# Kernel tuning notes

Measured on AMD Instinct MI355X. Metric: run time of the kernel, lower is better.

## Reference

```python
import jax, jax.numpy as jnp
import numpy as np


def _inside_mask(points, boxes3d):
    # points: (B, N, 3); boxes3d: (B, M, 7) = (cx, cy, cz_bottom, dx, dy, dz, rz)
    cx, cy, cz, dx, dy, dz, rz = [boxes3d[..., i] for i in range(7)]
    cz = cz + dz * 0.5  # bottom-center -> geometric center (mmcv convention)
    # shift into box frame: (B, M, N)
    sx = points[:, None, :, 0] - cx[..., None]
    sy = points[:, None, :, 1] - cy[..., None]
    sz = points[:, None, :, 2] - cz[..., None]
    cosa = jnp.cos(-rz)[..., None]
    sina = jnp.sin(-rz)[..., None]
    lx = sx * cosa - sy * sina
    ly = sx * sina + sy * cosa
    return (
        (jnp.abs(lx) < dx[..., None] * 0.5)
        & (jnp.abs(ly) < dy[..., None] * 0.5)
        & (jnp.abs(sz) <= dz[..., None] * 0.5)
    )


def setup_inputs() -> dict:
    key = jax.random.key(0)
    k1, k2, k3 = jax.random.split(key, 3)
    B, N, M, C = 4, 16384, 128, 128
    points = jax.random.uniform(k1, (B, N, 3), dtype=jnp.float32)
    point_features = jax.random.normal(k2, (B, N, C), dtype=jnp.float32)
    boxes3d = jax.random.uniform(k3, (B, M, 7), dtype=jnp.float32)
    return {
        "points": points,
        "point_features": point_features,
        "boxes3d": boxes3d,
        "num_sampled_points": 512,
    }


def reference(points, point_features, boxes3d, num_sampled_points):
    S = num_sampled_points
    mask = _inside_mask(points, boxes3d)            # (B, M, N) bool
    cnt = mask.sum(axis=-1)                          # (B, M)
    # stable sort brings inside-point indices first, in original order
    order = jnp.argsort((~mask).astype(jnp.int32), axis=-1, stable=True)  # (B, M, N)
    cnt_safe = jnp.maximum(cnt, 1)
    # CUDA kernel: sample index k maps to k % cnt (== k when k < cnt)
    sample_pos = jnp.arange(S, dtype=cnt.dtype)[None, None, :] % cnt_safe[..., None]
    idx = jnp.take_along_axis(order, sample_pos, axis=-1)  # (B, M, S)
    gathered_pts = jnp.take_along_axis(points[:, None], idx[..., None], axis=2)          # (B, M, S, 3)
    gathered_feat = jnp.take_along_axis(point_features[:, None], idx[..., None], axis=2)  # (B, M, S, C)
    pooled = jnp.concatenate([gathered_pts, gathered_feat], axis=-1)  # (B, M, S, 3+C)
    nonempty = (cnt > 0)
    pooled = pooled * nonempty[..., None, None].astype(pooled.dtype)
    empty_flag = (~nonempty).astype(jnp.int32)
    return pooled, empty_flag
```

## Files before the change

kernel.cpp:

```cpp
#include <hip/hip_runtime.h>
#include <hip/hip_bf16.h>

#define BB   4
#define NN   16384
#define MM   128
#define CC   128
#define SS   512
#define CH   (CC + 3)
#define BM   (BB * MM)
#define WAVES 4
#define CHUNK (NN / WAVES)

__global__ __launch_bounds__(256)
void box_sample_kernel(const float* __restrict__ points,
                       const float* __restrict__ boxes,
                       int*  __restrict__ idx_ws,
                       int*  __restrict__ cnt_ws,
                       float* __restrict__ flag_out)
{
    const int box  = blockIdx.x;
    const int b    = box >> 7;
    const int lane = threadIdx.x & 63;
    const int w    = threadIdx.x >> 6;

    const float* P  = points + (size_t)b * NN * 3;
    const float* bx = boxes  + (size_t)box * 7;

    const float cx = bx[0], cy = bx[1], cz = bx[2];
    const float dx = bx[3], dy = bx[4], dz = bx[5], rz = bx[6];

    const float  czc = cz + dz * 0.5f;
    const float  hz  = dz * 0.5f;
    const double ca  = cos(-(double)rz);
    const double sa  = sin(-(double)rz);
    const double hx  = (double)dx * 0.5;
    const double hy  = (double)dy * 0.5;

    __shared__ int s_part[WAVES][SS];
    __shared__ int s_cnt[WAVES];
    __shared__ int s_idx[SS];

    int cnt = 0;
    const int pbase = w * CHUNK;
    for (int i0 = 0; i0 < CHUNK; i0 += 64) {
        const int i = pbase + i0 + lane;
        const float px = P[i * 3 + 0];
        const float py = P[i * 3 + 1];
        const float pz = P[i * 3 + 2];

        const double sx = (double)px - (double)cx;
        const double sy = (double)py - (double)cy;
        const float  szf = pz - czc;

        const double lx = sx * ca - sy * sa;
        const double ly = sx * sa + sy * ca;

        const bool inside = (fabs(lx) < hx) && (fabs(ly) < hy) && (fabsf(szf) <= hz);

        const unsigned long long mask = __ballot(inside);
        const int pos = cnt + __popcll(mask & ((1ull << lane) - 1ull));
        if (inside && pos < SS) s_part[w][pos] = i;
        cnt += __popcll(mask);
        if (cnt >= SS) break;
    }
    if (lane == 0) s_cnt[w] = cnt;
    __syncthreads();

    const int c0 = s_cnt[0], c1 = s_cnt[1], c2 = s_cnt[2], c3 = s_cnt[3];
    const int o1 = c0, o2 = c0 + c1, o3 = c0 + c1 + c2;
    const int total = o3 + c3;

    for (int k = threadIdx.x; k < SS; k += 256) {
        int v = 0;
        if      (k < c0)    v = s_part[0][k];
        else if (k < o2)    v = s_part[1][k - o1];
        else if (k < o3)    v = s_part[2][k - o2];
        else if (k < total) v = s_part[3][k - o3];
        s_idx[k] = v;
    }
    __syncthreads();

    if (total > 0 && total < SS) {
        for (int k = total + threadIdx.x; k < SS; k += 256)
            s_idx[k] = s_idx[k % total];
        __syncthreads();
    }

    int* dst = idx_ws + (size_t)box * SS;
    for (int k = threadIdx.x; k < SS; k += 256) dst[k] = s_idx[k];
    if (threadIdx.x == 0) {
        cnt_ws[box]   = total;
        flag_out[box] = (total == 0) ? 1.0f : 0.0f;
    }
}

__global__ __launch_bounds__(256)
void gather_kernel(const float* __restrict__ points,
                   const float* __restrict__ feats,
                   const int*   __restrict__ idx_ws,
                   const int*   __restrict__ cnt_ws,
                   float* __restrict__ out)
{
    const int box   = blockIdx.x;
    const int chunk = blockIdx.y;
    const int b     = box >> 7;
    const int tid   = threadIdx.x;
    const int hw    = tid >> 5;
    const int j     = tid & 31;

    __shared__ int   s_idx[32];
    __shared__ float s_scale;
    if (tid < 32) s_idx[tid] = idx_ws[(size_t)box * SS + chunk * 32 + tid];
    if (tid == 0) s_scale = (cnt_ws[box] > 0) ? 1.0f : 0.0f;
    __syncthreads();
    const float scale = s_scale;

    const float4* F4 = (const float4*)(feats + (size_t)b * NN * CC);
    const float*  Pb = points + (size_t)b * NN * 3;
    float* dstbox = out + (size_t)box * SS * CH + (size_t)chunk * 32 * CH;

    #pragma unroll
    for (int s = 0; s < 4; ++s) {
        const int k   = hw + s * 8;
        const int idx = s_idx[k];
        const float4 v = F4[idx * 32 + j];
        float* d = dstbox + k * CH;
        d[3 + 4 * j + 0] = v.x * scale;
        d[3 + 4 * j + 1] = v.y * scale;
        d[3 + 4 * j + 2] = v.z * scale;
        d[3 + 4 * j + 3] = v.w * scale;
        if (j < 3) d[j] = Pb[idx * 3 + j] * scale;
    }
}

extern "C" void kernel_launch(void* const* d_in, const int* in_sizes, int n_in,
                              void* d_out, int out_size, void* d_ws, size_t ws_size,
                              hipStream_t stream) {
    const float* points = (const float*)d_in[0];
    const float* feats  = (const float*)d_in[1];
    const float* boxes  = (const float*)d_in[2];

    int*  idx_ws = (int*)d_ws;
    int*  cnt_ws = idx_ws + (size_t)BM * SS;
    float* out      = (float*)d_out;
    float* flag_out = out + (size_t)BM * SS * CH;

    box_sample_kernel<<<BM, 256, 0, stream>>>(points, boxes, idx_ws, cnt_ws, flag_out);
    dim3 ggrid(BM, SS / 32);
    gather_kernel<<<ggrid, 256, 0, stream>>>(points, feats, idx_ws, cnt_ws, out);
}
```

Measured before the change: 225.4 us.

## Stage gather output in LDS for float4 stores; widen and unroll box sampling

The gather kernel now assembles each 32-sample tile of 131-float rows in shared memory. It then writes the tile to global memory as contiguous float4 stores instead of scattered scalar stores at an odd row stride. This targets write efficiency on the large output tensor. The sampling kernel goes from 4 to 8 waves per box, unrolls the point loads four at a time, and drops the per-wave early exit, so each wave always scans its whole chunk in exchange for more memory-level parallelism.

```diff
diff --git a/kernel.cpp b/kernel.cpp
--- a/kernel.cpp
+++ b/kernel.cpp
@@ -8,10 +8,10 @@
 #define SS   512
 #define CH   (CC + 3)
 #define BM   (BB * MM)
-#define WAVES 4
+#define WAVES 8
 #define CHUNK (NN / WAVES)
 
-__global__ __launch_bounds__(256)
+__global__ __launch_bounds__(512)
 void box_sample_kernel(const float* __restrict__ points,
                        const float* __restrict__ boxes,
                        int*  __restrict__ idx_ws,
@@ -42,52 +42,56 @@
 
     int cnt = 0;
     const int pbase = w * CHUNK;
-    for (int i0 = 0; i0 < CHUNK; i0 += 64) {
-        const int i = pbase + i0 + lane;
-        const float px = P[i * 3 + 0];
-        const float py = P[i * 3 + 1];
-        const float pz = P[i * 3 + 2];
-
-        const double sx = (double)px - (double)cx;
-        const double sy = (double)py - (double)cy;
-        const float  szf = pz - czc;
-
-        const double lx = sx * ca - sy * sa;
-        const double ly = sx * sa + sy * ca;
-
-        const bool inside = (fabs(lx) < hx) && (fabs(ly) < hy) && (fabsf(szf) <= hz);
-
-        const unsigned long long mask = __ballot(inside);
-        const int pos = cnt + __popcll(mask & ((1ull << lane) - 1ull));
-        if (inside && pos < SS) s_part[w][pos] = i;
-        cnt += __popcll(mask);
-        if (cnt >= SS) break;
+    for (int i0 = 0; i0 < CHUNK; i0 += 256) {
+        float px[4], py[4], pz[4];
+        #pragma unroll
+        for (int u = 0; u < 4; ++u) {
+            const int i = pbase + i0 + u * 64 + lane;
+            px[u] = P[i * 3 + 0];
+            py[u] = P[i * 3 + 1];
+            pz[u] = P[i * 3 + 2];
+        }
+        #pragma unroll
+        for (int u = 0; u < 4; ++u) {
+            const double sx = (double)px[u] - (double)cx;
+            const double sy = (double)py[u] - (double)cy;
+            const float  szf = pz[u] - czc;
+            const double lx = sx * ca - sy * sa;
+            const double ly = sx * sa + sy * ca;
+            const bool inside = (fabs(lx) < hx) && (fabs(ly) < hy) && (fabsf(szf) <= hz);
+            const unsigned long long mask = __ballot(inside);
+            const int pos = cnt + __popcll(mask & ((1ull << lane) - 1ull));
+            if (inside && pos < SS) s_part[w][pos] = pbase + i0 + u * 64 + lane;
+            cnt += __popcll(mask);
+        }
     }
     if (lane == 0) s_cnt[w] = cnt;
     __syncthreads();
 
-    const int c0 = s_cnt[0], c1 = s_cnt[1], c2 = s_cnt[2], c3 = s_cnt[3];
-    const int o1 = c0, o2 = c0 + c1, o3 = c0 + c1 + c2;
-    const int total = o3 + c3;
+    int c[WAVES], off[WAVES];
+    int total = 0;
+    #pragma unroll
+    for (int q = 0; q < WAVES; ++q) { c[q] = s_cnt[q]; off[q] = total; total += c[q]; }
 
-    for (int k = threadIdx.x; k < SS; k += 256) {
+    for (int k = threadIdx.x; k < SS; k += 512) {
         int v = 0;
-        if      (k < c0)    v = s_part[0][k];
-        else if (k < o2)    v = s_part[1][k - o1];
-        else if (k < o3)    v = s_part[2][k - o2];
-        else if (k < total) v = s_part[3][k - o3];
+        #pragma unroll
+        for (int q = 0; q < WAVES; ++q) {
+            const int r = k - off[q];
+            if (r >= 0 && r < c[q]) v = s_part[q][r];
+        }
         s_idx[k] = v;
     }
     __syncthreads();
 
     if (total > 0 && total < SS) {
-        for (int k = total + threadIdx.x; k < SS; k += 256)
+        for (int k = total + threadIdx.x; k < SS; k += 512)
             s_idx[k] = s_idx[k % total];
         __syncthreads();
     }
 
     int* dst = idx_ws + (size_t)box * SS;
-    for (int k = threadIdx.x; k < SS; k += 256) dst[k] = s_idx[k];
+    for (int k = threadIdx.x; k < SS; k += 512) dst[k] = s_idx[k];
     if (threadIdx.x == 0) {
         cnt_ws[box]   = total;
         flag_out[box] = (total == 0) ? 1.0f : 0.0f;
@@ -110,6 +114,8 @@
 
     __shared__ int   s_idx[32];
     __shared__ float s_scale;
+    __shared__ __align__(16) float s_buf[32 * CH];
+
     if (tid < 32) s_idx[tid] = idx_ws[(size_t)box * SS + chunk * 32 + tid];
     if (tid == 0) s_scale = (cnt_ws[box] > 0) ? 1.0f : 0.0f;
     __syncthreads();
@@ -117,20 +123,26 @@
 
     const float4* F4 = (const float4*)(feats + (size_t)b * NN * CC);
     const float*  Pb = points + (size_t)b * NN * 3;
-    float* dstbox = out + (size_t)box * SS * CH + (size_t)chunk * 32 * CH;
 
     #pragma unroll
     for (int s = 0; s < 4; ++s) {
         const int k   = hw + s * 8;
         const int idx = s_idx[k];
         const float4 v = F4[idx * 32 + j];
-        float* d = dstbox + k * CH;
-        d[3 + 4 * j + 0] = v.x * scale;
-        d[3 + 4 * j + 1] = v.y * scale;
-        d[3 + 4 * j + 2] = v.z * scale;
-        d[3 + 4 * j + 3] = v.w * scale;
-        if (j < 3) d[j] = Pb[idx * 3 + j] * scale;
+        const int base = k * CH + 3 + 4 * j;
+        s_buf[base + 0] = v.x * scale;
+        s_buf[base + 1] = v.y * scale;
+        s_buf[base + 2] = v.z * scale;
+        s_buf[base + 3] = v.w * scale;
+        if (j < 3) s_buf[k * CH + j] = Pb[idx * 3 + j] * scale;
     }
+    __syncthreads();
+
+    const float4* src4 = (const float4*)s_buf;
+    float4* dst4 = (float4*)(out + (size_t)box * SS * CH + (size_t)chunk * 32 * CH);
+    #pragma unroll
+    for (int s = 0; s < 4; ++s) dst4[s * 256 + tid] = src4[s * 256 + tid];
+    if (tid < 24) dst4[1024 + tid] = src4[1024 + tid];
 }
 
 extern "C" void kernel_launch(void* const* d_in, const int* in_sizes, int n_in,
@@ -145,7 +157,7 @@
     float* out      = (float*)d_out;
     float* flag_out = out + (size_t)BM * SS * CH;
 
-    box_sample_kernel<<<BM, 256, 0, stream>>>(points, boxes, idx_ws, cnt_ws, flag_out);
+    box_sample_kernel<<<BM, 512, 0, stream>>>(points, boxes, idx_ws, cnt_ws, flag_out);
     dim3 ggrid(BM, SS / 32);
     gather_kernel<<<ggrid, 256, 0, stream>>>(points, feats, idx_ws, cnt_ws, out);
 }
```

Result: faster. 197.7 us (-12.3%).
